# Kernel optimization log

Hardware: AMD Instinct MI355X
Metric: run time of the kernel (lower is better)

## Reference

```python
import jax, jax.numpy as jnp
import numpy as np

FWD_TRUNCATION = 0.05
EPS_LOG = 1e-20


def setup_inputs() -> dict:
    key = jax.random.key(0)
    k1, k2, k3, k4, k5 = jax.random.split(key, 5)
    B, N, M = 32768, 1024, 64
    samples = jax.random.normal(k1, (B, M), dtype=jnp.float32)
    mask = jax.random.uniform(k2, (B, M), dtype=jnp.float32)
    centroids = jax.random.normal(k3, (N, M), dtype=jnp.float32)
    # sd kept away from 0 to avoid huge 1/sd scaling
    sd = jax.random.uniform(k4, (1, M), dtype=jnp.float32) + 0.5
    log_marginal = jax.random.normal(k5, (1, N), dtype=jnp.float32)
    return {"samples": samples, "mask": mask, "centroids": centroids,
            "sd": sd, "log_marginal": log_marginal}


def _masked_pairwise_sq_distances(A, B, mask):
    # A: [B, M] samples, B: [N, M] centroids, mask: [B, M]
    sq_mask = mask * mask
    mA = mask * A
    A_d = jnp.sum(mA * mA, axis=1, keepdims=True)            # [B, 1]
    B_d = sq_mask @ (B * B).T                                 # [B, N]
    cross = (sq_mask * A) @ B.T                                # [B, N]
    return jax.nn.relu(A_d - 2.0 * cross + B_d)               # [B, N]


def _pdf_truncate(pdf, truncation):
    # discretePdfTruncate: zero out entries below truncation * rowmax, renormalize
    threshold = truncation * jnp.max(pdf, axis=-1, keepdims=True)
    pdf = jax.nn.relu(jnp.sign(pdf - threshold)) * pdf
    return pdf / jnp.sum(pdf, axis=-1, keepdims=True)


def reference(samples, mask, centroids, sd, log_marginal):
    # Mahalanobis: fold 1/sd into the mask (sqMahalanobisDistances)
    m = mask / sd
    dist = _masked_pairwise_sq_distances(samples, centroids, m)  # [B, N]
    log_prior = jax.nn.log_softmax(log_marginal, axis=-1)        # [1, N]
    logits = log_prior - 0.5 * dist                              # [B, N]
    # softmaxWithTemperature (temperature=1) -> truncate -> renormalize
    pdf = jax.nn.softmax(logits, axis=-1)
    pdf = _pdf_truncate(pdf, FWD_TRUNCATION)
    log_pdf = jnp.log(pdf + EPS_LOG)                             # logPdfTruncate
    return pdf, log_pdf
```

## Files before the change

### kernel.cpp

```cpp
#include <hip/hip_runtime.h>
#include <math.h>

#define N_C 1024
#define M_F 64
#define B_R 32768
#define R_B 16
#define LDX 132
#define PF  3

typedef short bf16x8 __attribute__((ext_vector_type(8)));
typedef float f32x4 __attribute__((ext_vector_type(4)));
typedef unsigned int uint4v __attribute__((ext_vector_type(4)));

__device__ __forceinline__ short f2bf(float x) {
  unsigned b = __float_as_uint(x);
  b += 0x7fffu + ((b >> 16) & 1u);
  return (short)(b >> 16);
}
__device__ __forceinline__ float bf2f(short h) {
  return __uint_as_float(((unsigned)(unsigned short)h) << 16);
}

__device__ __forceinline__ void split3(const float* f, bf16x8& h, bf16x8& m, bf16x8& l) {
  uint4v hp, mp, lp;
#pragma unroll
  for (int i = 0; i < 4; ++i) {
    const unsigned b0 = __float_as_uint(f[2 * i]);
    const unsigned b1 = __float_as_uint(f[2 * i + 1]);
    const unsigned h0 = b0 & 0xFFFF0000u, h1 = b1 & 0xFFFF0000u;
    const float r0 = f[2 * i] - __uint_as_float(h0);
    const float r1 = f[2 * i + 1] - __uint_as_float(h1);
    hp[i] = (b0 >> 16) | h1;
    const unsigned rb0 = __float_as_uint(r0), rb1 = __float_as_uint(r1);
    const unsigned m0 = rb0 & 0xFFFF0000u, m1 = rb1 & 0xFFFF0000u;
    const float s0 = r0 - __uint_as_float(m0);
    const float s1 = r1 - __uint_as_float(m1);
    mp[i] = (rb0 >> 16) | m1;
    lp[i] = (__float_as_uint(s0) >> 16) | (__float_as_uint(s1) & 0xFFFF0000u);
  }
  h = __builtin_bit_cast(bf16x8, hp);
  m = __builtin_bit_cast(bf16x8, mp);
  l = __builtin_bit_cast(bf16x8, lp);
}

__global__ void logprior_kernel(const float* __restrict__ lm, float* __restrict__ lp) {
  __shared__ float red[256];
  const int t = threadIdx.x;
  float v[4];
  float mx = -INFINITY;
#pragma unroll
  for (int i = 0; i < 4; ++i) { v[i] = lm[i * 256 + t]; mx = fmaxf(mx, v[i]); }
  red[t] = mx;
  __syncthreads();
  for (int s = 128; s > 0; s >>= 1) {
    if (t < s) red[t] = fmaxf(red[t], red[t + s]);
    __syncthreads();
  }
  mx = red[0];
  __syncthreads();
  float sum = 0.f;
#pragma unroll
  for (int i = 0; i < 4; ++i) { v[i] -= mx; sum += expf(v[i]); }
  red[t] = sum;
  __syncthreads();
  for (int s = 128; s > 0; s >>= 1) {
    if (t < s) red[t] += red[t + s];
    __syncthreads();
  }
  const float l = logf(red[0]);
#pragma unroll
  for (int i = 0; i < 4; ++i) lp[i * 256 + t] = v[i] - l;
}

__global__ void prep_y(const float* __restrict__ centroids,
                       bf16x8* __restrict__ yh, bf16x8* __restrict__ ym,
                       bf16x8* __restrict__ yl) {
  const int tid = blockIdx.x * 256 + threadIdx.x;
  const int l = tid & 63;
  const int c = (tid >> 6) & 63;
  const int s = tid >> 12;
  const int n = c * 16 + (l & 15);
  const int k0 = s * 32 + (l >> 4) * 8;
  bf16x8 h, mid, lo;
#pragma unroll
  for (int j = 0; j < 8; ++j) {
    const int k = k0 + j;
    float y;
    if (k < 64) {
      y = centroids[n * M_F + k];
    } else {
      const float cc = centroids[n * M_F + (k - 64)];
      y = cc * cc;
    }
    const short hh = f2bf(y);
    const float r1 = y - bf2f(hh);
    const short mm = f2bf(r1);
    const float r2 = r1 - bf2f(mm);
    h[j] = hh;
    mid[j] = mm;
    lo[j] = f2bf(r2);
  }
  const int blob = (s * 64 + c) * 64 + l;
  yh[blob] = h;
  ym[blob] = mid;
  yl[blob] = lo;
}

__global__ __launch_bounds__(256, 3) void rmm_main(
    const float* __restrict__ samples, const float* __restrict__ mask,
    const float* __restrict__ sd, const float* __restrict__ lp_g,
    const bf16x8* __restrict__ yh_g, const bf16x8* __restrict__ ym_g,
    const bf16x8* __restrict__ yl_g, float* __restrict__ out) {
  __shared__ float xs[R_B * LDX];
  __shared__ float lp_s[N_C];
  __shared__ float ad_s[R_B];
  __shared__ float red_s[R_B * 4];

  const int t = threadIdx.x;
  const int b0 = blockIdx.x * R_B;
  const int w = t >> 6;
  const int l = t & 63;
  const int m = l & 15;
  const int q = l >> 4;

  *(float4*)(lp_s + (t << 2)) = *(const float4*)(lp_g + (t << 2));

  {
    const int r = t >> 4;
    const int j4 = (t & 15) << 2;
    const float4 s4 = *(const float4*)(samples + (size_t)(b0 + r) * M_F + j4);
    const float4 m4 = *(const float4*)(mask + (size_t)(b0 + r) * M_F + j4);
    const float4 d4 = *(const float4*)(sd + j4);
    const float sa[4] = {s4.x, s4.y, s4.z, s4.w};
    const float ma[4] = {m4.x, m4.y, m4.z, m4.w};
    const float da[4] = {d4.x, d4.y, d4.z, d4.w};
    float ad = 0.f;
#pragma unroll
    for (int k = 0; k < 4; ++k) {
      const float mm = ma[k] / da[k];
      const float uu = mm * mm;
      const float mA = mm * sa[k];
      ad = fmaf(mA, mA, ad);
      xs[r * LDX + j4 + k] = -2.0f * (uu * sa[k]);
      xs[r * LDX + 64 + j4 + k] = uu;
    }
#pragma unroll
    for (int off = 1; off < 16; off <<= 1) ad += __shfl_xor(ad, off, 64);
    if ((t & 15) == 0) ad_s[r] = ad;
  }

  f32x4 acc[16];
#pragma unroll
  for (int c = 0; c < 16; ++c) acc[c] = (f32x4){0.f, 0.f, 0.f, 0.f};

  __syncthreads();

#pragma unroll 1
  for (int s = 0; s < 4; ++s) {
    const size_t sbase = (size_t)(s * 64 + w * 16) * 64 + l;
    const bf16x8* yh = yh_g + sbase;
    const bf16x8* ym = ym_g + sbase;
    const bf16x8* yl = yl_g + sbase;

    bf16x8 Bh[PF], Bm[PF], Bl[PF];
#pragma unroll
    for (int p = 0; p < PF; ++p) {
      Bh[p] = yh[p * 64];
      Bm[p] = ym[p * 64];
      Bl[p] = yl[p * 64];
    }

    const float* xp = &xs[m * LDX + s * 32 + q * 8];
    float av[8];
    *(float4*)&av[0] = *(const float4*)xp;
    *(float4*)&av[4] = *(const float4*)(xp + 4);
    bf16x8 ah, am, al;
    split3(av, ah, am, al);

#pragma unroll
    for (int c = 0; c < 16; ++c) {
      const int cur = c % PF;
      const bf16x8 bh = Bh[cur], bm = Bm[cur], bl = Bl[cur];
      if (c + PF < 16) {
        Bh[cur] = yh[(c + PF) * 64];
        Bm[cur] = ym[(c + PF) * 64];
        Bl[cur] = yl[(c + PF) * 64];
      }
      acc[c] = __builtin_amdgcn_mfma_f32_16x16x32_bf16(am, bl, acc[c], 0, 0, 0);
      acc[c] = __builtin_amdgcn_mfma_f32_16x16x32_bf16(al, bm, acc[c], 0, 0, 0);
      acc[c] = __builtin_amdgcn_mfma_f32_16x16x32_bf16(ah, bl, acc[c], 0, 0, 0);
      acc[c] = __builtin_amdgcn_mfma_f32_16x16x32_bf16(am, bm, acc[c], 0, 0, 0);
      acc[c] = __builtin_amdgcn_mfma_f32_16x16x32_bf16(al, bh, acc[c], 0, 0, 0);
      acc[c] = __builtin_amdgcn_mfma_f32_16x16x32_bf16(ah, bm, acc[c], 0, 0, 0);
      acc[c] = __builtin_amdgcn_mfma_f32_16x16x32_bf16(am, bh, acc[c], 0, 0, 0);
      acc[c] = __builtin_amdgcn_mfma_f32_16x16x32_bf16(ah, bh, acc[c], 0, 0, 0);
    }
  }

  float adv[4];
#pragma unroll
  for (int g = 0; g < 4; ++g) adv[g] = ad_s[q * 4 + g];
  float lpv[16];
#pragma unroll
  for (int c = 0; c < 16; ++c) lpv[c] = lp_s[w * 256 + c * 16 + m];

#pragma unroll
  for (int c = 0; c < 16; ++c)
#pragma unroll
    for (int g = 0; g < 4; ++g) {
      const float dist = fmaxf(adv[g] + acc[c][g], 0.0f);
      acc[c][g] = lpv[c] - 0.5f * dist;
    }

  float mx[4];
#pragma unroll
  for (int g = 0; g < 4; ++g) {
    float v = acc[0][g];
#pragma unroll
    for (int c = 1; c < 16; ++c) v = fmaxf(v, acc[c][g]);
#pragma unroll
    for (int off = 1; off < 16; off <<= 1) v = fmaxf(v, __shfl_xor(v, off, 64));
    mx[g] = v;
  }
  if (m == 0) {
#pragma unroll
    for (int g = 0; g < 4; ++g) red_s[(q * 4 + g) * 4 + w] = mx[g];
  }
  __syncthreads();
#pragma unroll
  for (int g = 0; g < 4; ++g) {
    const float4 rv = *(const float4*)(&red_s[(q * 4 + g) * 4]);
    mx[g] = fmaxf(fmaxf(rv.x, rv.y), fmaxf(rv.z, rv.w));
  }
  __syncthreads();

  float sm[4];
#pragma unroll
  for (int g = 0; g < 4; ++g) {
    float ssum = 0.f;
#pragma unroll
    for (int c = 0; c < 16; ++c) {
      const float e = __expf(acc[c][g] - mx[g]);
      acc[c][g] = e;
      ssum += e;
    }
#pragma unroll
    for (int off = 1; off < 16; off <<= 1) ssum += __shfl_xor(ssum, off, 64);
    sm[g] = ssum;
  }
  if (m == 0) {
#pragma unroll
    for (int g = 0; g < 4; ++g) red_s[(q * 4 + g) * 4 + w] = sm[g];
  }
  __syncthreads();
#pragma unroll
  for (int g = 0; g < 4; ++g) {
    const float4 rv = *(const float4*)(&red_s[(q * 4 + g) * 4]);
    sm[g] = (rv.x + rv.y) + (rv.z + rv.w);
  }
  __syncthreads();

  float thr[4], qs[4];
#pragma unroll
  for (int g = 0; g < 4; ++g) {
    const float S1 = sm[g];
    thr[g] = 0.05f * (1.0f / S1);
    float s2 = 0.f;
#pragma unroll
    for (int c = 0; c < 16; ++c) {
      const float p = acc[c][g] / S1;
      acc[c][g] = p;
      s2 += (p > thr[g]) ? p : 0.0f;
    }
#pragma unroll
    for (int off = 1; off < 16; off <<= 1) s2 += __shfl_xor(s2, off, 64);
    qs[g] = s2;
  }
  if (m == 0) {
#pragma unroll
    for (int g = 0; g < 4; ++g) red_s[(q * 4 + g) * 4 + w] = qs[g];
  }
  __syncthreads();
#pragma unroll
  for (int g = 0; g < 4; ++g) {
    const float4 rv = *(const float4*)(&red_s[(q * 4 + g) * 4]);
    qs[g] = (rv.x + rv.y) + (rv.z + rv.w);
  }

  const size_t colbase = (size_t)(w * 256 + m);
#pragma unroll
  for (int g = 0; g < 4; ++g) {
    const float rq = 1.0f / qs[g];
    float* orow = out + (size_t)(b0 + q * 4 + g) * N_C + colbase;
    float* lrow = orow + (size_t)B_R * N_C;
#pragma unroll
    for (int c = 0; c < 16; ++c) {
      const float p = acc[c][g];
      const float pf = (p > thr[g]) ? (p * rq) : 0.0f;
      orow[c * 16] = pf;
      lrow[c * 16] = __logf(pf + 1e-20f);
    }
  }
}

extern "C" void kernel_launch(void* const* d_in, const int* in_sizes, int n_in,
                              void* d_out, int out_size, void* d_ws, size_t ws_size,
                              hipStream_t stream) {
  const float* samples   = (const float*)d_in[0];
  const float* mask      = (const float*)d_in[1];
  const float* centroids = (const float*)d_in[2];
  const float* sd        = (const float*)d_in[3];
  const float* lm        = (const float*)d_in[4];
  float* out = (float*)d_out;

  char* ws = (char*)d_ws;
  float* lp  = (float*)ws;
  bf16x8* yh = (bf16x8*)(ws + 4096);
  bf16x8* ym = (bf16x8*)(ws + 4096 + 262144);
  bf16x8* yl = (bf16x8*)(ws + 4096 + 2 * 262144);

  logprior_kernel<<<1, 256, 0, stream>>>(lm, lp);
  prep_y<<<64, 256, 0, stream>>>(centroids, yh, ym, yl);
  rmm_main<<<B_R / R_B, 256, 0, stream>>>(samples, mask, sd, lp, yh, ym, yl, out);
}
```

Baseline: 344.5 us.

## Interleave bf16 split planes per tile and prefetch continuously across K-steps

The hi/mid/lo bf16 planes of the centroid operand are interleaved per tile into one buffer, so each tile's three fragments sit next to each other in memory. The register prefetch ring now runs across all four K-steps instead of restarting and stalling at each step boundary. Prefetch depth drops from 3 to 2 and launch bounds rise from 3 to 4 waves per EU to free registers for more occupancy. The shallower prefetch may expose more load latency if the added occupancy does not hide it.

Result: slower. 354.0 us (+2.8%).

```diff
diff --git a/kernel.cpp b/kernel.cpp
--- a/kernel.cpp
+++ b/kernel.cpp
@@ -6,7 +6,7 @@
 #define B_R 32768
 #define R_B 16
 #define LDX 132
-#define PF  3
+#define PF  2
 
 typedef short bf16x8 __attribute__((ext_vector_type(8)));
 typedef float f32x4 __attribute__((ext_vector_type(4)));
@@ -72,9 +72,7 @@
   for (int i = 0; i < 4; ++i) lp[i * 256 + t] = v[i] - l;
 }
 
-__global__ void prep_y(const float* __restrict__ centroids,
-                       bf16x8* __restrict__ yh, bf16x8* __restrict__ ym,
-                       bf16x8* __restrict__ yl) {
+__global__ void prep_y(const float* __restrict__ centroids, bf16x8* __restrict__ yb) {
   const int tid = blockIdx.x * 256 + threadIdx.x;
   const int l = tid & 63;
   const int c = (tid >> 6) & 63;
@@ -100,17 +98,16 @@
     mid[j] = mm;
     lo[j] = f2bf(r2);
   }
-  const int blob = (s * 64 + c) * 64 + l;
-  yh[blob] = h;
-  ym[blob] = mid;
-  yl[blob] = lo;
-}
-
-__global__ __launch_bounds__(256, 3) void rmm_main(
+  const int tile = s * 64 + c;
+  yb[(size_t)(tile * 3 + 0) * 64 + l] = h;
+  yb[(size_t)(tile * 3 + 1) * 64 + l] = mid;
+  yb[(size_t)(tile * 3 + 2) * 64 + l] = lo;
+}
+
+__global__ __launch_bounds__(256, 4) void rmm_main(
     const float* __restrict__ samples, const float* __restrict__ mask,
     const float* __restrict__ sd, const float* __restrict__ lp_g,
-    const bf16x8* __restrict__ yh_g, const bf16x8* __restrict__ ym_g,
-    const bf16x8* __restrict__ yl_g, float* __restrict__ out) {
+    const bf16x8* __restrict__ yb_g, float* __restrict__ out) {
   __shared__ float xs[R_B * LDX];
   __shared__ float lp_s[N_C];
   __shared__ float ad_s[R_B];
@@ -155,36 +152,39 @@
 
   __syncthreads();
 
+  const bf16x8* yb = yb_g + l;
+
+  bf16x8 Bh[PF], Bm[PF], Bl[PF];
+#pragma unroll
+  for (int p = 0; p < PF; ++p) {
+    const int g = w * 16 + p;
+    Bh[p] = yb[(size_t)(g * 3 + 0) * 64];
+    Bm[p] = yb[(size_t)(g * 3 + 1) * 64];
+    Bl[p] = yb[(size_t)(g * 3 + 2) * 64];
+  }
+
+  bf16x8 ah, am, al;
+
 #pragma unroll 1
   for (int s = 0; s < 4; ++s) {
-    const size_t sbase = (size_t)(s * 64 + w * 16) * 64 + l;
-    const bf16x8* yh = yh_g + sbase;
-    const bf16x8* ym = ym_g + sbase;
-    const bf16x8* yl = yl_g + sbase;
-
-    bf16x8 Bh[PF], Bm[PF], Bl[PF];
-#pragma unroll
-    for (int p = 0; p < PF; ++p) {
-      Bh[p] = yh[p * 64];
-      Bm[p] = ym[p * 64];
-      Bl[p] = yl[p * 64];
-    }
-
-    const float* xp = &xs[m * LDX + s * 32 + q * 8];
-    float av[8];
-    *(float4*)&av[0] = *(const float4*)xp;
-    *(float4*)&av[4] = *(const float4*)(xp + 4);
-    bf16x8 ah, am, al;
-    split3(av, ah, am, al);
+    {
+      const float* xp = &xs[m * LDX + s * 32 + q * 8];
+      float av[8];
+      *(float4*)&av[0] = *(const float4*)xp;
+      *(float4*)&av[4] = *(const float4*)(xp + 4);
+      split3(av, ah, am, al);
+    }
 
 #pragma unroll
     for (int c = 0; c < 16; ++c) {
-      const int cur = c % PF;
+      const int cur = (s * 16 + c) & (PF - 1);
       const bf16x8 bh = Bh[cur], bm = Bm[cur], bl = Bl[cur];
-      if (c + PF < 16) {
-        Bh[cur] = yh[(c + PF) * 64];
-        Bm[cur] = ym[(c + PF) * 64];
-        Bl[cur] = yl[(c + PF) * 64];
+      const int tcr = s * 16 + c + PF;
+      if (tcr < 64) {
+        const int gr = (tcr >> 4) * 64 + w * 16 + (tcr & 15);
+        Bh[cur] = yb[(size_t)(gr * 3 + 0) * 64];
+        Bm[cur] = yb[(size_t)(gr * 3 + 1) * 64];
+        Bl[cur] = yb[(size_t)(gr * 3 + 2) * 64];
       }
       acc[c] = __builtin_amdgcn_mfma_f32_16x16x32_bf16(am, bl, acc[c], 0, 0, 0);
       acc[c] = __builtin_amdgcn_mfma_f32_16x16x32_bf16(al, bm, acc[c], 0, 0, 0);
@@ -315,11 +315,9 @@
 
   char* ws = (char*)d_ws;
   float* lp  = (float*)ws;
-  bf16x8* yh = (bf16x8*)(ws + 4096);
-  bf16x8* ym = (bf16x8*)(ws + 4096 + 262144);
-  bf16x8* yl = (bf16x8*)(ws + 4096 + 2 * 262144);
+  bf16x8* yb = (bf16x8*)(ws + 4096);
 
   logprior_kernel<<<1, 256, 0, stream>>>(lm, lp);
-  prep_y<<<64, 256, 0, stream>>>(centroids, yh, ym, yl);
-  rmm_main<<<B_R / R_B, 256, 0, stream>>>(samples, mask, sd, lp, yh, ym, yl, out);
-}
+  prep_y<<<64, 256, 0, stream>>>(centroids, yb);
+  rmm_main<<<B_R / R_B, 256, 0, stream>>>(samples, mask, sd, lp, yb, out);
+}
```
